# Kernel tuning notes

Measured on AMD Instinct MI355X. Metric: run time of the kernel, lower is better.

## Reference

```python
import jax, jax.numpy as jnp
import numpy as np

IN_SHAPE = (128, 128, 128)   # (d, w, h)
RES_SCALE = 1.5
SCAN_RANGE = 11.0
PROJ_NUM = 4
SPACING = np.array([1.0, 1.0, 1.0])
OUT_SHAPE = (256, 256)
BATCH = 2


def _make_grids():
    # Faithful numpy port of proj_layer._project_grid_multi (precomputed buffers).
    d, w, h = IN_SHAPE
    p = PROJ_NUM
    half = SCAN_RANGE / 2.0
    poses = np.zeros((p, 3))
    poses[:, 1] = 3.0
    poses[:, 0] = np.tan(np.linspace(-half, half, p) / 180.0 * np.pi) * 3.0
    poses[:, 2] = np.linspace(-0.2, 0.2, p)
    emi = poses * w                                  # emitter positions, (p,3)
    res_d, res_h = int(d * RES_SCALE), int(h * RES_SCALE)
    Nvec = np.array([0.0, 1.0, 0.0])
    P0 = np.linspace(0, w - 1, w)[:, None] * np.array([[0.0, 1.0, 0.0]])  # (w,3)
    lin_x = np.linspace(-res_d / 2, res_d / 2 - 1, res_d)
    lin_y = np.linspace(-res_h / 2, res_h / 2 - 1, res_h)
    gx, gy = np.meshgrid(lin_x, lin_y, indexing='ij')
    I = np.stack([gx, np.zeros_like(gx), gy], axis=-1)   # (rd,rh,3) detector plane
    I = I[None] - emi[:, None, None, :]                  # (p,rd,rh,3) ray dirs
    dxr = I / I[..., 1:2]
    In = I / np.linalg.norm(I, axis=3, keepdims=True)
    dxr = np.linalg.norm(dxr * SPACING[None, None, None, :], axis=3)  # (p,rd,rh) step length
    inv_IN = 1.0 / (In @ Nvec)                           # (p,rd,rh)
    PN = (P0[None] - emi[:, None, :]) @ Nvec             # (p,w)
    T = inv_IN[..., None] * PN[:, None, None, :]         # (p,rd,rh,w) ray params
    grid = In[..., None, :] * T[..., None] + emi[:, None, None, None, :]  # (p,rd,rh,w,3)
    gn = np.empty_like(grid)
    gn[..., 0] = grid[..., 0] / d * 2.0
    gn[..., 1] = grid[..., 1] / w * 2.0 - 1.0
    gn[..., 2] = grid[..., 2] / h * 2.0
    gn = gn[..., ::-1]  # torch.flip(grid, [4]) -> grid_sample (x,y,z) order
    return np.ascontiguousarray(gn).astype(np.float32), dxr.astype(np.float32)


def setup_inputs() -> dict:
    key = jax.random.key(0)
    x = jax.random.normal(key, (BATCH,) + IN_SHAPE, dtype=jnp.float32)
    g, dxr = _make_grids()
    return {"x": x, "grids": jnp.asarray(g), "dx": jnp.asarray(dxr)}


def _trilinear_gather(vol, coords):
    # vol: (b, D, H, W); coords: (N,3) normalized [-1,1], (x,y,z) -> (W,H,D)
    # F.grid_sample(mode='bilinear', padding_mode='zeros', align_corners=True)
    b, D, H, W = vol.shape
    ix = (coords[:, 0] + 1.0) * 0.5 * (W - 1)
    iy = (coords[:, 1] + 1.0) * 0.5 * (H - 1)
    iz = (coords[:, 2] + 1.0) * 0.5 * (D - 1)
    x0, y0, z0 = jnp.floor(ix), jnp.floor(iy), jnp.floor(iz)
    fx, fy, fz = ix - x0, iy - y0, iz - z0
    volf = vol.reshape(b, -1)
    out = jnp.zeros((b, coords.shape[0]), vol.dtype)
    for dz in (0, 1):
        wz = fz if dz else 1.0 - fz
        zi = z0 + dz
        for dy in (0, 1):
            wy = fy if dy else 1.0 - fy
            yi = y0 + dy
            for dxx in (0, 1):
                wx = fx if dxx else 1.0 - fx
                xi = x0 + dxx
                valid = ((xi >= 0) & (xi <= W - 1) & (yi >= 0) & (yi <= H - 1)
                         & (zi >= 0) & (zi <= D - 1))
                idx = ((jnp.clip(zi, 0, D - 1).astype(jnp.int32) * H
                        + jnp.clip(yi, 0, H - 1).astype(jnp.int32)) * W
                       + jnp.clip(xi, 0, W - 1).astype(jnp.int32))
                wgt = jnp.where(valid, wx * wy * wz, 0.0)
                out = out + volf[:, idx] * wgt[None, :]
    return out


def _nearest_resize(t, out_hw):
    # F.interpolate(mode='nearest'): src = floor(dst * in / out)
    b, c, H, W = t.shape
    oh, ow = out_hw
    hi = jnp.minimum((jnp.arange(oh) * H) // oh, H - 1)
    wi = jnp.minimum((jnp.arange(ow) * W) // ow, W - 1)
    return t[:, :, hi][:, :, :, wi]


def reference(x, grids, dx):
    p, rd, rh, w = grids.shape[:4]
    b = x.shape[0]
    coords = grids.reshape(-1, 3)                       # (p*rd*rh*w, 3)
    samples = _trilinear_gather(x, coords).reshape(b, p, rd, rh, w)
    x_proj = samples.sum(axis=4) * dx[None]             # ray-sum projection
    return _nearest_resize(x_proj, OUT_SHAPE)
```

## Files before the change

### kernel.cpp

```cpp
#include <hip/hip_runtime.h>
#include <hip/hip_bf16.h>

#define PNUM 4
#define RD   192
#define RH   192
#define OHH  256
#define OWW  256
#define NB   2
#define ROWS (PNUM * RD * RH)
#define VOL  (128 * 128 * 128)
#define WSPL 8

typedef float        vf4 __attribute__((ext_vector_type(4)));
typedef float        vf2 __attribute__((ext_vector_type(2)));
typedef unsigned int vu2 __attribute__((ext_vector_type(2)));

__device__ __forceinline__ unsigned int bf16_bits(float f) {
    __hip_bfloat16 h = __float2bfloat16(f);
    return (unsigned int)__hip_bfloat16_raw(h).x;
}
__device__ __forceinline__ float hi_bits_f(unsigned int u) {
    u &= 0xffff0000u;
    return __builtin_bit_cast(float, u);
}
__device__ __forceinline__ float lo_bits_f(unsigned int u) {
    u <<= 16;
    return __builtin_bit_cast(float, u);
}


__global__ __launch_bounds__(256) void ray_setup_kernel(
    const float* __restrict__ grids,
    float* __restrict__ rayp,
    float* __restrict__ zp)
{
    const int ray = (int)(blockIdx.x * 256 + threadIdx.x);
    const float* g = grids + (size_t)ray * 384;
    const vf4 L0 = *(const vf4*)g;
    const vf4 L1 = *(const vf4*)(g + 192);
    vf2 r;
    r.x = (L0.x + 1.f) * 63.5f;
    r.y = (L1.x - L0.x) * 0.9921875f;
    *(vf2*)(rayp + (size_t)ray * 2) = r;
    if ((ray % RH) == 0) {
        vf2 z;
        z.x = (L0.z + 1.f) * 63.5f;
        z.y = (L1.z - L0.z) * 0.9921875f;
        *(vf2*)(zp + (size_t)(ray / RH) * 2) = z;
    }
}

__global__ __launch_bounds__(256) void ycomb_kernel(
    const float* __restrict__ x,
    vu2* __restrict__ ycomb)
{
    const int i  = (int)(blockIdx.x * 256 + threadIdx.x);
    const int w  = i >> 14;
    const int z  = (i >> 7) & 127;
    const int xc = i & 127;

    const float WY0 = (float)w * 0.0078125f;
    const float WY1 = 1.f - WY0;
    const int   rm  = (w > 0) ? (w - 1) : 0;

    const int b0 = (z * 128 + rm) * 128;
    const int b1 = (z * 128 + w) * 128;
    const int x1 = (xc < 127) ? (xc + 1) : 127;

    const float a0 = fmaf(WY0, x[b0 + xc],       WY1 * x[b1 + xc]);
    const float a1 = fmaf(WY0, x[VOL + b0 + xc], WY1 * x[VOL + b1 + xc]);
    const float c0 = fmaf(WY0, x[b0 + x1],       WY1 * x[b1 + x1]);
    const float c1 = fmaf(WY0, x[VOL + b0 + x1], WY1 * x[VOL + b1 + x1]);

    vu2 q;
    q.x = bf16_bits(a0) | (bf16_bits(a1) << 16);
    q.y = bf16_bits(c0) | (bf16_bits(c1) << 16);
    ycomb[i] = q;
}

__global__ __launch_bounds__(256, 8) void proj_kernel(
    const vu2*  __restrict__ ycomb,
    const float* __restrict__ rayp,
    const float* __restrict__ zp,
    float* __restrict__ part)
{
    const int b    = (int)blockIdx.x;
    const int rdp  = b / 6;
    const int rem  = b % 6;
    const int t    = rem >> 1;
    const int h    = rem & 1;
    const int wave = (int)threadIdx.x >> 6;
    const int lane = (int)threadIdx.x & 63;
    const int wc   = h * 4 + wave;
    const int ray  = rdp * RH + t * 64 + lane;

    const vf2 xp = *(const vf2*)(rayp + (size_t)ray * 2);
    const vf2 zv = *(const vf2*)(zp + (size_t)rdp * 2);

    float s0 = 0.f, s1 = 0.f;
    const int wbase = wc * 16;

#pragma unroll 4
    for (int wu = 0; wu < 16; ++wu) {
        const int   w  = wbase + wu;
        const float wf = (float)w;
        const float ix = fmaf(wf, xp.y, xp.x);
        const float iz = fmaf(wf, zv.y, zv.x);

        const float xf = floorf(ix);
        const float fx = ix - xf;
        const int   xb = (int)xf;
        const int   xl = min(max(xb, 0), 126);
        const bool  inx = (xb >= 0) && (xb <= 126);
        const float WL = inx ? (1.f - fx) : ((xb == -1)  ? fx         : 0.f);
        const float WR = inx ? fx         : ((xb == 127) ? (1.f - fx) : 0.f);

        const float zf = floorf(iz);
        const float fz = iz - zf;
        const int   zb  = (int)zf;
        const int   zi0 = min(max(zb,     0), 127);
        const int   zi1 = min(max(zb + 1, 0), 127);
        const float WZ0 = (zb >= 0  && zb <= 127) ? (1.f - fz) : 0.f;
        const float WZ1 = (zb >= -1 && zb <= 126) ? fz         : 0.f;

        const int base = w << 14;
        const vu2 q0 = ycomb[base + (zi0 << 7) + xl];
        const vu2 q1 = ycomb[base + (zi1 << 7) + xl];

        const float v00 = fmaf(WL, lo_bits_f(q0.x), WR * lo_bits_f(q0.y));
        const float v01 = fmaf(WL, hi_bits_f(q0.x), WR * hi_bits_f(q0.y));
        const float v10 = fmaf(WL, lo_bits_f(q1.x), WR * lo_bits_f(q1.y));
        const float v11 = fmaf(WL, hi_bits_f(q1.x), WR * hi_bits_f(q1.y));

        s0 = fmaf(WZ0, v00, fmaf(WZ1, v10, s0));
        s1 = fmaf(WZ0, v01, fmaf(WZ1, v11, s1));
    }

    part[((size_t)wc * NB + 0) * ROWS + ray] = s0;
    part[((size_t)wc * NB + 1) * ROWS + ray] = s1;
}


__global__ __launch_bounds__(256) void proj_rays_fb_kernel(
    const float* __restrict__ x,
    const float* __restrict__ grids,
    float* __restrict__ part)
{
    const int tid  = (int)(blockIdx.x * blockDim.x + threadIdx.x);
    const int wave = tid >> 6;
    const int lane = tid & 63;
    const int wcc  = wave & 3;
    const int rr   = wave >> 2;
    const int ray  = rr * 64 + lane;

    const float* g  = grids + (size_t)ray * 384 + wcc * 96;
    const float* v0 = x;
    const float* v1 = x + VOL;

    float s0 = 0.f, s1 = 0.f;
    for (int w0 = 0; w0 < 32; w0 += 16) {
        const vf4* gc = (const vf4*)(g + w0 * 3);
        float cf[48];
#pragma unroll
        for (int i = 0; i < 12; ++i) {
            const vf4 t = gc[i];
            cf[4*i+0] = t.x; cf[4*i+1] = t.y; cf[4*i+2] = t.z; cf[4*i+3] = t.w;
        }
#pragma unroll
        for (int w = 0; w < 16; ++w) {
            const float ix = (cf[3*w+0] + 1.f) * 63.5f;
            const float iy = (cf[3*w+1] + 1.f) * 63.5f;
            const float iz = (cf[3*w+2] + 1.f) * 63.5f;
            const float x0f = floorf(ix), y0f = floorf(iy), z0f = floorf(iz);
            const float fxx = ix - x0f, fyy = iy - y0f, fzz = iz - z0f;
            const float wx0 = (x0f >= 0.f && x0f <= 127.f) ? (1.f-fxx) : 0.f;
            const float wx1 = (x0f+1.f >= 0.f && x0f+1.f <= 127.f) ? fxx : 0.f;
            const float wy0 = (y0f >= 0.f && y0f <= 127.f) ? (1.f-fyy) : 0.f;
            const float wy1 = (y0f+1.f >= 0.f && y0f+1.f <= 127.f) ? fyy : 0.f;
            const float wz0 = (z0f >= 0.f && z0f <= 127.f) ? (1.f-fzz) : 0.f;
            const float wz1 = (z0f+1.f >= 0.f && z0f+1.f <= 127.f) ? fzz : 0.f;
            const int xi0 = (int)fminf(fmaxf(x0f,0.f),127.f);
            const int xi1 = (int)fminf(fmaxf(x0f+1.f,0.f),127.f);
            const int yi0 = (int)fminf(fmaxf(y0f,0.f),127.f);
            const int yi1 = (int)fminf(fmaxf(y0f+1.f,0.f),127.f);
            const int zi0 = (int)fminf(fmaxf(z0f,0.f),127.f);
            const int zi1 = (int)fminf(fmaxf(z0f+1.f,0.f),127.f);
            const int b00 = (zi0*128+yi0)*128, b01 = (zi0*128+yi1)*128;
            const int b10 = (zi1*128+yi0)*128, b11 = (zi1*128+yi1)*128;
            const float w000 = wz0*wy0*wx0, w001 = wz0*wy0*wx1;
            const float w010 = wz0*wy1*wx0, w011 = wz0*wy1*wx1;
            const float w100 = wz1*wy0*wx0, w101 = wz1*wy0*wx1;
            const float w110 = wz1*wy1*wx0, w111 = wz1*wy1*wx1;
            s0 += w000*v0[b00+xi0] + w001*v0[b00+xi1] + w010*v0[b01+xi0] + w011*v0[b01+xi1]
                + w100*v0[b10+xi0] + w101*v0[b10+xi1] + w110*v0[b11+xi0] + w111*v0[b11+xi1];
            s1 += w000*v1[b00+xi0] + w001*v1[b00+xi1] + w010*v1[b01+xi0] + w011*v1[b01+xi1]
                + w100*v1[b10+xi0] + w101*v1[b10+xi1] + w110*v1[b11+xi0] + w111*v1[b11+xi1];
        }
    }
    part[((size_t)wcc * NB + 0) * ROWS + ray] = s0;
    part[((size_t)wcc * NB + 1) * ROWS + ray] = s1;
}


__global__ __launch_bounds__(256) void resize_reduce_kernel(
    const float* __restrict__ part,
    const float* __restrict__ dx,
    float* __restrict__ out,
    int wsplit)
{
    const int idx = (int)(blockIdx.x * blockDim.x + threadIdx.x);
    const int ow = idx & (OWW - 1);
    const int oh = (idx >> 8) & (OHH - 1);
    const int bp = idx >> 16;
    const int b  = bp >> 2;
    const int p  = bp & 3;
    const int hi = (oh * 3) >> 2;
    const int wi = (ow * 3) >> 2;
    const int ray = (p * RD + hi) * RH + wi;

    float s = 0.f;
    for (int wcc = 0; wcc < wsplit; ++wcc)
        s += part[((size_t)wcc * NB + b) * ROWS + ray];
    out[idx] = s * dx[ray];
}

extern "C" void kernel_launch(void* const* d_in, const int* in_sizes, int n_in,
                              void* d_out, int out_size, void* d_ws, size_t ws_size,
                              hipStream_t stream) {
    const float* x     = (const float*)d_in[0];
    const float* grids = (const float*)d_in[1];
    const float* dx    = (const float*)d_in[2];
    float* out = (float*)d_out;
    char*  ws  = (char*)d_ws;

    const size_t YC_B   = (size_t)VOL * 8;
    const size_t RAYP_B = (size_t)ROWS * 2 * 4;
    const size_t ZP_B   = (size_t)PNUM * RD * 2 * 4;
    const size_t PART_B = (size_t)WSPL * NB * ROWS * 4;
    const size_t NEED   = YC_B + RAYP_B + ZP_B + PART_B;

    if (ws_size >= NEED) {
        vu2*   ycomb = (vu2*)ws;
        float* rayp  = (float*)(ws + YC_B);
        float* zp    = (float*)(ws + YC_B + RAYP_B);
        float* part  = (float*)(ws + YC_B + RAYP_B + ZP_B);

        ray_setup_kernel<<<ROWS / 256, 256, 0, stream>>>(grids, rayp, zp);
        ycomb_kernel    <<<VOL / 256, 256, 0, stream>>>(x, ycomb);
        proj_kernel     <<<(PNUM * RD) * 3 * 2, 256, 0, stream>>>(ycomb, rayp, zp, part);
        resize_reduce_kernel<<<(NB * PNUM * OHH * OWW) / 256, 256, 0, stream>>>(part, dx, out, WSPL);
    } else {
        float* part = (float*)ws;
        proj_rays_fb_kernel<<<ROWS * 4 / 256, 256, 0, stream>>>(x, grids, part);
        resize_reduce_kernel<<<(NB * PNUM * OHH * OWW) / 256, 256, 0, stream>>>(part, dx, out, 4);
    }
}
```

Baseline: 310.4 us.

## Stage shared z-rows in LDS with prefetch and cut the w-split to two

```diff
diff --git a/kernel.cpp b/kernel.cpp
--- a/kernel.cpp
+++ b/kernel.cpp
@@ -9,11 +9,12 @@
 #define NB   2
 #define ROWS (PNUM * RD * RH)
 #define VOL  (128 * 128 * 128)
-#define WSPL 8
+#define WSPL 2
 
 typedef float        vf4 __attribute__((ext_vector_type(4)));
 typedef float        vf2 __attribute__((ext_vector_type(2)));
 typedef unsigned int vu2 __attribute__((ext_vector_type(2)));
+typedef unsigned int vu4 __attribute__((ext_vector_type(4)));
 
 __device__ __forceinline__ unsigned int bf16_bits(float f) {
     __hip_bfloat16 h = __float2bfloat16(f);
@@ -78,35 +79,63 @@
     ycomb[i] = q;
 }
 
-__global__ __launch_bounds__(256, 8) void proj_kernel(
+__global__ __launch_bounds__(128) void proj_kernel(
     const vu2*  __restrict__ ycomb,
     const float* __restrict__ rayp,
     const float* __restrict__ zp,
     float* __restrict__ part)
 {
+    __shared__ __align__(16) vu2 lds[2][2][2][128];
+
     const int b    = (int)blockIdx.x;
-    const int rdp  = b / 6;
-    const int rem  = b % 6;
-    const int t    = rem >> 1;
-    const int h    = rem & 1;
-    const int wave = (int)threadIdx.x >> 6;
+    const int rdp  = b / 3;
+    const int t    = b % 3;
+    const int h    = (int)threadIdx.x >> 6;
     const int lane = (int)threadIdx.x & 63;
-    const int wc   = h * 4 + wave;
     const int ray  = rdp * RH + t * 64 + lane;
 
     const vf2 xp = *(const vf2*)(rayp + (size_t)ray * 2);
     const vf2 zv = *(const vf2*)(zp + (size_t)rdp * 2);
 
+    const int wbase = h * 64;
+
+    auto zrows = [&](int w, int& zi0, int& zi1, float& WZ0, float& WZ1) {
+        const float iz = fmaf((float)w, zv.y, zv.x);
+        const float zf = floorf(iz);
+        const float fz = iz - zf;
+        const int   zb = (int)zf;
+        zi0 = min(max(zb,     0), 127);
+        zi1 = min(max(zb + 1, 0), 127);
+        WZ0 = (zb >= 0  && zb <= 127) ? (1.f - fz) : 0.f;
+        WZ1 = (zb >= -1 && zb <= 126) ? fz         : 0.f;
+    };
+
     float s0 = 0.f, s1 = 0.f;
-    const int wbase = wc * 16;
-
-#pragma unroll 4
-    for (int wu = 0; wu < 16; ++wu) {
-        const int   w  = wbase + wu;
-        const float wf = (float)w;
+    float WZ0, WZ1, nWZ0, nWZ1;
+    int   zi0, zi1, nzi0, nzi1;
+
+    zrows(wbase, zi0, zi1, WZ0, WZ1);
+    {
+        const vu4* r0 = (const vu4*)(ycomb + ((size_t)wbase << 14) + (zi0 << 7));
+        const vu4* r1 = (const vu4*)(ycomb + ((size_t)wbase << 14) + (zi1 << 7));
+        ((vu4*)&lds[h][0][0][0])[lane] = r0[lane];
+        ((vu4*)&lds[h][0][1][0])[lane] = r1[lane];
+    }
+
+#pragma unroll 2
+    for (int wu = 0; wu < 64; ++wu) {
+        const int   w   = wbase + wu;
+        const int   buf = wu & 1;
+        const float wf  = (float)w;
+
+        const int wn = (wu < 63) ? (w + 1) : w;
+        zrows(wn, nzi0, nzi1, nWZ0, nWZ1);
+        const vu4* r0 = (const vu4*)(ycomb + ((size_t)wn << 14) + (nzi0 << 7));
+        const vu4* r1 = (const vu4*)(ycomb + ((size_t)wn << 14) + (nzi1 << 7));
+        const vu4 t0 = r0[lane];
+        const vu4 t1 = r1[lane];
+
         const float ix = fmaf(wf, xp.y, xp.x);
-        const float iz = fmaf(wf, zv.y, zv.x);
-
         const float xf = floorf(ix);
         const float fx = ix - xf;
         const int   xb = (int)xf;
@@ -115,17 +144,8 @@
         const float WL = inx ? (1.f - fx) : ((xb == -1)  ? fx         : 0.f);
         const float WR = inx ? fx         : ((xb == 127) ? (1.f - fx) : 0.f);
 
-        const float zf = floorf(iz);
-        const float fz = iz - zf;
-        const int   zb  = (int)zf;
-        const int   zi0 = min(max(zb,     0), 127);
-        const int   zi1 = min(max(zb + 1, 0), 127);
-        const float WZ0 = (zb >= 0  && zb <= 127) ? (1.f - fz) : 0.f;
-        const float WZ1 = (zb >= -1 && zb <= 126) ? fz         : 0.f;
-
-        const int base = w << 14;
-        const vu2 q0 = ycomb[base + (zi0 << 7) + xl];
-        const vu2 q1 = ycomb[base + (zi1 << 7) + xl];
+        const vu2 q0 = lds[h][buf][0][xl];
+        const vu2 q1 = lds[h][buf][1][xl];
 
         const float v00 = fmaf(WL, lo_bits_f(q0.x), WR * lo_bits_f(q0.y));
         const float v01 = fmaf(WL, hi_bits_f(q0.x), WR * hi_bits_f(q0.y));
@@ -134,10 +154,15 @@
 
         s0 = fmaf(WZ0, v00, fmaf(WZ1, v10, s0));
         s1 = fmaf(WZ0, v01, fmaf(WZ1, v11, s1));
-    }
-
-    part[((size_t)wc * NB + 0) * ROWS + ray] = s0;
-    part[((size_t)wc * NB + 1) * ROWS + ray] = s1;
+
+        ((vu4*)&lds[h][buf ^ 1][0][0])[lane] = t0;
+        ((vu4*)&lds[h][buf ^ 1][1][0])[lane] = t1;
+
+        zi0 = nzi0; zi1 = nzi1; WZ0 = nWZ0; WZ1 = nWZ1;
+    }
+
+    part[((size_t)h * NB + 0) * ROWS + ray] = s0;
+    part[((size_t)h * NB + 1) * ROWS + ray] = s1;
 }
 
 
@@ -247,7 +272,7 @@
 
         ray_setup_kernel<<<ROWS / 256, 256, 0, stream>>>(grids, rayp, zp);
         ycomb_kernel    <<<VOL / 256, 256, 0, stream>>>(x, ycomb);
-        proj_kernel     <<<(PNUM * RD) * 3 * 2, 256, 0, stream>>>(ycomb, rayp, zp, part);
+        proj_kernel     <<<(PNUM * RD) * 3, 128, 0, stream>>>(ycomb, rayp, zp, part);
         resize_reduce_kernel<<<(NB * PNUM * OHH * OWW) / 256, 256, 0, stream>>>(part, dx, out, WSPL);
     } else {
         float* part = (float*)ws;
```

Measured after the change: 317.7 us. +2.3%, slower.

## Stage ycomb rows in double-buffered LDS and drop w-split partial sums

Applied to the files above, without the earlier changes.

```diff
diff --git a/kernel.cpp b/kernel.cpp
--- a/kernel.cpp
+++ b/kernel.cpp
@@ -9,11 +9,11 @@
 #define NB   2
 #define ROWS (PNUM * RD * RH)
 #define VOL  (128 * 128 * 128)
-#define WSPL 8
 
 typedef float        vf4 __attribute__((ext_vector_type(4)));
 typedef float        vf2 __attribute__((ext_vector_type(2)));
 typedef unsigned int vu2 __attribute__((ext_vector_type(2)));
+typedef unsigned int vu4 __attribute__((ext_vector_type(4)));
 
 __device__ __forceinline__ unsigned int bf16_bits(float f) {
     __hip_bfloat16 h = __float2bfloat16(f);
@@ -78,66 +78,116 @@
     ycomb[i] = q;
 }
 
-__global__ __launch_bounds__(256, 8) void proj_kernel(
+__global__ __launch_bounds__(256) void proj_kernel(
     const vu2*  __restrict__ ycomb,
     const float* __restrict__ rayp,
     const float* __restrict__ zp,
     float* __restrict__ part)
 {
-    const int b    = (int)blockIdx.x;
-    const int rdp  = b / 6;
-    const int rem  = b % 6;
-    const int t    = rem >> 1;
-    const int h    = rem & 1;
-    const int wave = (int)threadIdx.x >> 6;
-    const int lane = (int)threadIdx.x & 63;
-    const int wc   = h * 4 + wave;
-    const int ray  = rdp * RH + t * 64 + lane;
-
-    const vf2 xp = *(const vf2*)(rayp + (size_t)ray * 2);
+    __shared__ __align__(16) vu2 lds[2][8][2][128];
+
+    const int orig = (int)blockIdx.x;
+    const int rdp  = (orig & 7) * (PNUM * RD / 8) + (orig >> 3);
+
+    const int tid  = (int)threadIdx.x;
+    const int wv   = tid >> 6;
+    const int lane = tid & 63;
+
     const vf2 zv = *(const vf2*)(zp + (size_t)rdp * 2);
 
+    const int  ray   = rdp * RH + wv * 64 + lane;
+    const bool comp  = (wv < 3);
+    vf2 xp = {0.f, 0.f};
+    if (comp) xp = *(const vf2*)(rayp + (size_t)ray * 2);
+
+    auto row_src = [&](int wb, int p) -> const vu4* {
+        const int row = 4 * p + wv;
+        const int wi  = row >> 1;
+        const int zr  = row & 1;
+        const int w   = wb + wi;
+        const float iz = fmaf((float)w, zv.y, zv.x);
+        const int   zb = (int)floorf(iz);
+        const int   zi = zr ? min(max(zb + 1, 0), 127) : min(max(zb, 0), 127);
+        return (const vu4*)(ycomb + ((size_t)w << 14) + ((size_t)zi << 7));
+    };
+
+    {
+        const vu4 t0 = row_src(0, 0)[lane];
+        const vu4 t1 = row_src(0, 1)[lane];
+        const vu4 t2 = row_src(0, 2)[lane];
+        const vu4 t3 = row_src(0, 3)[lane];
+        ((vu4*)&lds[0][(4*0+wv)>>1][(4*0+wv)&1][0])[lane] = t0;
+        ((vu4*)&lds[0][(4*1+wv)>>1][(4*1+wv)&1][0])[lane] = t1;
+        ((vu4*)&lds[0][(4*2+wv)>>1][(4*2+wv)&1][0])[lane] = t2;
+        ((vu4*)&lds[0][(4*3+wv)>>1][(4*3+wv)&1][0])[lane] = t3;
+    }
+    __syncthreads();
+
     float s0 = 0.f, s1 = 0.f;
-    const int wbase = wc * 16;
-
-#pragma unroll 4
-    for (int wu = 0; wu < 16; ++wu) {
-        const int   w  = wbase + wu;
-        const float wf = (float)w;
-        const float ix = fmaf(wf, xp.y, xp.x);
-        const float iz = fmaf(wf, zv.y, zv.x);
-
-        const float xf = floorf(ix);
-        const float fx = ix - xf;
-        const int   xb = (int)xf;
-        const int   xl = min(max(xb, 0), 126);
-        const bool  inx = (xb >= 0) && (xb <= 126);
-        const float WL = inx ? (1.f - fx) : ((xb == -1)  ? fx         : 0.f);
-        const float WR = inx ? fx         : ((xb == 127) ? (1.f - fx) : 0.f);
-
-        const float zf = floorf(iz);
-        const float fz = iz - zf;
-        const int   zb  = (int)zf;
-        const int   zi0 = min(max(zb,     0), 127);
-        const int   zi1 = min(max(zb + 1, 0), 127);
-        const float WZ0 = (zb >= 0  && zb <= 127) ? (1.f - fz) : 0.f;
-        const float WZ1 = (zb >= -1 && zb <= 126) ? fz         : 0.f;
-
-        const int base = w << 14;
-        const vu2 q0 = ycomb[base + (zi0 << 7) + xl];
-        const vu2 q1 = ycomb[base + (zi1 << 7) + xl];
-
-        const float v00 = fmaf(WL, lo_bits_f(q0.x), WR * lo_bits_f(q0.y));
-        const float v01 = fmaf(WL, hi_bits_f(q0.x), WR * hi_bits_f(q0.y));
-        const float v10 = fmaf(WL, lo_bits_f(q1.x), WR * lo_bits_f(q1.y));
-        const float v11 = fmaf(WL, hi_bits_f(q1.x), WR * hi_bits_f(q1.y));
-
-        s0 = fmaf(WZ0, v00, fmaf(WZ1, v10, s0));
-        s1 = fmaf(WZ0, v01, fmaf(WZ1, v11, s1));
-    }
-
-    part[((size_t)wc * NB + 0) * ROWS + ray] = s0;
-    part[((size_t)wc * NB + 1) * ROWS + ray] = s1;
+
+    for (int c = 0; c < 16; ++c) {
+        const int  buf = c & 1;
+        const int  wb  = c * 8;
+        const bool pre = (c < 15);
+
+        vu4 t0, t1, t2, t3;
+        if (pre) {
+            t0 = row_src(wb + 8, 0)[lane];
+            t1 = row_src(wb + 8, 1)[lane];
+            t2 = row_src(wb + 8, 2)[lane];
+            t3 = row_src(wb + 8, 3)[lane];
+        }
+
+        if (comp) {
+#pragma unroll
+            for (int wu = 0; wu < 8; ++wu) {
+                const int   w  = wb + wu;
+                const float wf = (float)w;
+                const float ix = fmaf(wf, xp.y, xp.x);
+                const float iz = fmaf(wf, zv.y, zv.x);
+
+                const float xf = floorf(ix);
+                const float fx = ix - xf;
+                const int   xb = (int)xf;
+                const int   xl = min(max(xb, 0), 126);
+                const bool  inx = (xb >= 0) && (xb <= 126);
+                const float WL = inx ? (1.f - fx) : ((xb == -1)  ? fx         : 0.f);
+                const float WR = inx ? fx         : ((xb == 127) ? (1.f - fx) : 0.f);
+
+                const float zf = floorf(iz);
+                const float fz = iz - zf;
+                const int   zb = (int)zf;
+                const float WZ0 = (zb >= 0  && zb <= 127) ? (1.f - fz) : 0.f;
+                const float WZ1 = (zb >= -1 && zb <= 126) ? fz         : 0.f;
+
+                const vu2 q0 = lds[buf][wu][0][xl];
+                const vu2 q1 = lds[buf][wu][1][xl];
+
+                const float v00 = fmaf(WL, lo_bits_f(q0.x), WR * lo_bits_f(q0.y));
+                const float v01 = fmaf(WL, hi_bits_f(q0.x), WR * hi_bits_f(q0.y));
+                const float v10 = fmaf(WL, lo_bits_f(q1.x), WR * lo_bits_f(q1.y));
+                const float v11 = fmaf(WL, hi_bits_f(q1.x), WR * hi_bits_f(q1.y));
+
+                s0 = fmaf(WZ0, v00, fmaf(WZ1, v10, s0));
+                s1 = fmaf(WZ0, v01, fmaf(WZ1, v11, s1));
+            }
+        }
+
+        if (pre) {
+            const int nb = buf ^ 1;
+            ((vu4*)&lds[nb][(4*0+wv)>>1][(4*0+wv)&1][0])[lane] = t0;
+            ((vu4*)&lds[nb][(4*1+wv)>>1][(4*1+wv)&1][0])[lane] = t1;
+            ((vu4*)&lds[nb][(4*2+wv)>>1][(4*2+wv)&1][0])[lane] = t2;
+            ((vu4*)&lds[nb][(4*3+wv)>>1][(4*3+wv)&1][0])[lane] = t3;
+        }
+
+        __syncthreads();
+    }
+
+    if (comp) {
+        part[ray]        = s0;
+        part[ROWS + ray] = s1;
+    }
 }
 
 
@@ -236,7 +286,7 @@
     const size_t YC_B   = (size_t)VOL * 8;
     const size_t RAYP_B = (size_t)ROWS * 2 * 4;
     const size_t ZP_B   = (size_t)PNUM * RD * 2 * 4;
-    const size_t PART_B = (size_t)WSPL * NB * ROWS * 4;
+    const size_t PART_B = (size_t)NB * ROWS * 4;
     const size_t NEED   = YC_B + RAYP_B + ZP_B + PART_B;
 
     if (ws_size >= NEED) {
@@ -247,8 +297,8 @@
 
         ray_setup_kernel<<<ROWS / 256, 256, 0, stream>>>(grids, rayp, zp);
         ycomb_kernel    <<<VOL / 256, 256, 0, stream>>>(x, ycomb);
-        proj_kernel     <<<(PNUM * RD) * 3 * 2, 256, 0, stream>>>(ycomb, rayp, zp, part);
-        resize_reduce_kernel<<<(NB * PNUM * OHH * OWW) / 256, 256, 0, stream>>>(part, dx, out, WSPL);
+        proj_kernel     <<<PNUM * RD, 256, 0, stream>>>(ycomb, rayp, zp, part);
+        resize_reduce_kernel<<<(NB * PNUM * OHH * OWW) / 256, 256, 0, stream>>>(part, dx, out, 1);
     } else {
         float* part = (float*)ws;
         proj_rays_fb_kernel<<<ROWS * 4 / 256, 256, 0, stream>>>(x, grids, part);
```

Measured after the change: 316.9 us. 2.1% more time.
